# Performance work log

Measured on AMD Instinct MI355X. Metric: run time of the kernel, lower is better.

Reference implementation:

```python
import jax, jax.numpy as jnp
import numpy as np

N = 20000   # nodes
E = 200000  # edges
D = 32      # inp_dim == out_dim == emb_dim
R = 100     # num_rel
EPS = 1e-5  # BatchNorm1d default eps


def setup_inputs() -> dict:
    key = jax.random.key(0)
    ks = jax.random.split(key, 5)
    h = jax.random.normal(ks[0], (N, D), dtype=jnp.float32)
    # xavier_uniform-ish scale for [R, D, D] relation weights
    weight = jax.random.normal(ks[1], (R, D, D), dtype=jnp.float32) * (1.0 / np.sqrt(D))
    gamma = jnp.ones((D,), dtype=jnp.float32)
    beta = jnp.zeros((D,), dtype=jnp.float32)
    src = jax.random.randint(ks[2], (E,), 0, N, dtype=jnp.int32)
    dst = jax.random.randint(ks[3], (E,), 0, N, dtype=jnp.int32)
    etype = jax.random.randint(ks[4], (E,), 0, R, dtype=jnp.int32)
    return {"h": h, "weight": weight, "gamma": gamma, "beta": beta,
            "src": src, "dst": dst, "etype": etype}


def reference(h, weight, gamma, beta, src, dst, etype):
    # per-edge relation-weight gather: [E, D, D]
    w_e = weight[etype]
    # per-edge bmm (src feature row-vector @ relation matrix) + relu: [E, D]
    msg = jax.nn.relu(jnp.einsum('ed,edo->eo', h[src], w_e))
    # BatchNorm1d in training mode: batch stats over the edge dimension
    mu = jnp.mean(msg, axis=0)
    var = jnp.mean(jnp.square(msg - mu), axis=0)  # biased variance
    msg = (msg - mu) * jax.lax.rsqrt(var + EPS) * gamma + beta
    # segment-mean reduce of messages into destination nodes: [N, D]
    ssum = jax.ops.segment_sum(msg, dst, num_segments=N)
    cnt = jax.ops.segment_sum(jnp.ones((E,), msg.dtype), dst, num_segments=N)
    return ssum / jnp.maximum(cnt, 1.0)[:, None]
```

## Files before the change

### kernel.cpp

```cpp
#include <hip/hip_runtime.h>

#define D 32
#define EPS 1e-5f
#define TPB 256
#define NB 256
#define RNB_MAX 25600
#define SCAN_T 1024

__global__ void histE_kernel(const int* __restrict__ etype, const int* __restrict__ dst,
                             int E, int R, int chunk,
                             int* __restrict__ blockHistT,
                             int* __restrict__ nodeCnt)
{
    __shared__ int lh[1024];
    for (int i = threadIdx.x; i < R; i += TPB) lh[i] = 0;
    __syncthreads();
    const int lo = blockIdx.x * chunk, hi = min(E, lo + chunk);
    for (int e = lo + threadIdx.x; e < hi; e += TPB) {
        atomicAdd(&lh[etype[e]], 1);
        atomicAdd(&nodeCnt[dst[e]], 1);
    }
    __syncthreads();
    for (int r = threadIdx.x; r < R; r += TPB)
        blockHistT[r * NB + blockIdx.x] = lh[r];
}

__global__ __launch_bounds__(SCAN_T)
void scanAll_kernel(int* __restrict__ blockHistT, int R,
                    const int* __restrict__ nodeCnt, int N, int E,
                    int* __restrict__ rel_start,
                    int* __restrict__ task_rel, int* __restrict__ task_start,
                    int* __restrict__ n_tasks,
                    int* __restrict__ node_start, int* __restrict__ curD)
{
    __shared__ int s_buf[RNB_MAX];
    __shared__ int s_part[SCAN_T];
    __shared__ int s_tbase[1024];
    const int t = threadIdx.x;

    const int M = R * NB;
    for (int i = t; i < M; i += SCAN_T) s_buf[i] = blockHistT[i];
    __syncthreads();
    {
        const int per = (M + SCAN_T - 1) / SCAN_T;
        const int lo = min(t * per, M), hi = min(lo + per, M);
        int s = 0;
        for (int i = lo; i < hi; ++i) s += s_buf[i];
        s_part[t] = s;
        __syncthreads();
        int x = s;
        for (int off = 1; off < SCAN_T; off <<= 1) {
            const int y = (t >= off) ? s_part[t - off] : 0;
            __syncthreads();
            x += y;
            s_part[t] = x;
            __syncthreads();
        }
        int run = x - s;
        for (int i = lo; i < hi; ++i) { const int v = s_buf[i]; s_buf[i] = run; run += v; }
    }
    __syncthreads();
    for (int i = t; i < M; i += SCAN_T) blockHistT[i] = s_buf[i];
    for (int r = t; r < R; r += SCAN_T) rel_start[r] = s_buf[r * NB];
    if (t == 0) rel_start[R] = E;
    if (t == 0) {
        int tb = 0;
        for (int r = 0; r < R; ++r) {
            const int st  = s_buf[r * NB];
            const int en  = (r + 1 < R) ? s_buf[(r + 1) * NB] : E;
            s_tbase[r] = tb;
            tb += (en - st + TPB - 1) / TPB;
        }
        *n_tasks = tb;
    }
    __syncthreads();
    if (t < R) {
        const int st = s_buf[t * NB];
        const int en = (t + 1 < R) ? s_buf[(t + 1) * NB] : E;
        const int nb = (en - st + TPB - 1) / TPB;
        const int tb = s_tbase[t];
        for (int b = 0; b < nb; ++b) {
            task_rel[tb + b]   = t;
            task_start[tb + b] = st + b * TPB;
        }
    }
    __syncthreads();

    for (int i = t; i < N; i += SCAN_T) s_buf[i] = nodeCnt[i];
    __syncthreads();
    {
        const int per = (N + SCAN_T - 1) / SCAN_T;
        const int lo = min(t * per, N), hi = min(lo + per, N);
        int s = 0;
        for (int i = lo; i < hi; ++i) s += s_buf[i];
        s_part[t] = s;
        __syncthreads();
        int x = s;
        for (int off = 1; off < SCAN_T; off <<= 1) {
            const int y = (t >= off) ? s_part[t - off] : 0;
            __syncthreads();
            x += y;
            s_part[t] = x;
            __syncthreads();
        }
        int run = x - s;
        for (int i = lo; i < hi; ++i) { const int v = s_buf[i]; s_buf[i] = run; run += v; }
    }
    __syncthreads();
    for (int i = t; i < N; i += SCAN_T) {
        const int v = s_buf[i];
        node_start[i] = v;
        curD[i] = v;
    }
    if (t == 0) node_start[N] = E;
}

__global__ void scatterE_kernel(const int* __restrict__ src, const int* __restrict__ dst,
                                const int* __restrict__ etype, int E, int R, int chunk,
                                const int* __restrict__ blockHistT,
                                int* __restrict__ ssrc, int* __restrict__ sdst)
{
    __shared__ int cur[1024];
    for (int r = threadIdx.x; r < R; r += TPB)
        cur[r] = blockHistT[r * NB + blockIdx.x];
    __syncthreads();
    const int lo = blockIdx.x * chunk, hi = min(E, lo + chunk);
    for (int e = lo + threadIdx.x; e < hi; e += TPB) {
        const int p = atomicAdd(&cur[etype[e]], 1);
        ssrc[p] = src[e];
        sdst[p] = dst[e];
    }
}

__global__ __launch_bounds__(TPB)
void rgcn_compute(const float* __restrict__ h, const float* __restrict__ W,
                  const int* __restrict__ rel_start,
                  const int* __restrict__ task_rel, const int* __restrict__ task_start,
                  const int* __restrict__ n_tasks_p,
                  const int* __restrict__ ssrc, const int* __restrict__ sdst,
                  int* __restrict__ curD,
                  float* __restrict__ msg,
                  float* __restrict__ stat_sum, float* __restrict__ stat_sq)
{
    __shared__ float s_tile[TPB * 33];
    __shared__ int   s_src[TPB];
    __shared__ int   s_pos[TPB];
    __shared__ float s_aux[2 * TPB];

    const int task = blockIdx.x;
    if (task >= *n_tasks_p) return;
    const int r      = task_rel[task];
    const int start  = task_start[task];
    const int relEnd = rel_start[r + 1];
    const int nE     = min(TPB, relEnd - start);
    const int tid    = threadIdx.x;

    if (tid < nE) {
        s_src[tid] = ssrc[start + tid];
        s_pos[tid] = atomicAdd(&curD[sdst[start + tid]], 1);
    }
    __syncthreads();

    for (int i = tid; i < nE * 8; i += TPB) {
        const int row = i >> 3, seg = i & 7;
        const float4 v = *(const float4*)(h + (size_t)s_src[row] * D + seg * 4);
        float* p = &s_tile[row * 33 + seg * 4];
        p[0] = v.x; p[1] = v.y; p[2] = v.z; p[3] = v.w;
    }
    __syncthreads();

    const float* Wr = W + (size_t)__builtin_amdgcn_readfirstlane(r) * (D * D);

    float acc[D];
#pragma unroll
    for (int o = 0; o < D; ++o) acc[o] = 0.f;

    if (tid < nE) {
#pragma unroll 4
        for (int d = 0; d < D; ++d) {
            const float hd = s_tile[tid * 33 + d];
#pragma unroll
            for (int o = 0; o < D; ++o)
                acc[o] = fmaf(hd, Wr[d * D + o], acc[o]);
        }
#pragma unroll
        for (int o = 0; o < D; ++o) acc[o] = fmaxf(acc[o], 0.f);
    }
    __syncthreads();

    if (tid < nE) {
#pragma unroll
        for (int o = 0; o < D; ++o) s_tile[tid * 33 + o] = acc[o];
    }
    __syncthreads();

    float ps = 0.f, pq = 0.f;
    for (int i = tid; i < nE * D; i += TPB) {
        const int row = i >> 5, o = i & 31;
        const float v = s_tile[row * 33 + o];
        msg[(size_t)s_pos[row] * D + o] = v;
        ps += v; pq += v * v;
    }
    s_aux[tid]       = ps;
    s_aux[TPB + tid] = pq;
    __syncthreads();
    if (tid < D) {
        float ss = 0.f, sq = 0.f;
#pragma unroll
        for (int c = 0; c < TPB / D; ++c) {
            ss += s_aux[c * D + tid];
            sq += s_aux[TPB + c * D + tid];
        }
        atomicAdd(&stat_sum[tid], ss);
        atomicAdd(&stat_sq[tid],  sq);
    }
}

__global__ void reduce_kernel(const float* __restrict__ msg,
                              const int* __restrict__ node_start,
                              const float* __restrict__ stat_sum,
                              const float* __restrict__ stat_sq,
                              const float* __restrict__ gamma,
                              const float* __restrict__ beta,
                              float invE, float* __restrict__ out, int N)
{
    const int o = threadIdx.x & 31;
    const int n = blockIdx.x * 8 + (threadIdx.x >> 5);
    if (n >= N) return;
    const int j0 = node_start[n], j1 = node_start[n + 1];
    float s = 0.f;
    for (int j = j0; j < j1; ++j)
        s += msg[(size_t)j * D + o];
    const float mu  = stat_sum[o] * invE;
    const float var = fmaxf(stat_sq[o] * invE - mu * mu, 0.f);
    const float is  = rsqrtf(var + EPS);
    const float sc  = gamma[o] * is;
    const float sh  = fmaf(-mu, sc, beta[o]);
    const float c   = (float)(j1 - j0);
    out[(size_t)n * D + o] = fmaf(s, sc, sh * c) / fmaxf(c, 1.0f);
}

extern "C" void kernel_launch(void* const* d_in, const int* in_sizes, int n_in,
                              void* d_out, int out_size, void* d_ws, size_t ws_size,
                              hipStream_t stream)
{
    const float* h     = (const float*)d_in[0];
    const float* W     = (const float*)d_in[1];
    const float* gamma = (const float*)d_in[2];
    const float* beta  = (const float*)d_in[3];
    const int*   src   = (const int*)d_in[4];
    const int*   dst   = (const int*)d_in[5];
    const int*   etype = (const int*)d_in[6];
    float* out = (float*)d_out;

    const int E = in_sizes[4];
    const int N = in_sizes[0] / D;
    const int R = in_sizes[1] / (D * D);
    const int T = R + (E + TPB - 1) / TPB;
    const int chunk = (E + NB - 1) / NB;

    int*   nodeCnt   = (int*)d_ws;
    float* stat_sum  = (float*)(nodeCnt + N);
    float* stat_sq   = stat_sum + D;
    int*   node_start= (int*)(stat_sq + D);
    int*   curD      = node_start + N + 1;
    int*   rel_start = curD + N;
    int*   n_tasks   = rel_start + R + 1;
    int*   blockHistT= n_tasks + 1;
    int*   task_rel  = blockHistT + R * NB;
    int*   task_start= task_rel + T;
    int*   ssrc      = task_start + T;
    int*   sdst      = ssrc + E;
    float* msg       = (float*)(sdst + E);

    hipMemsetAsync(d_ws, 0, sizeof(int) * (size_t)(N + 2 * D), stream);

    histE_kernel<<<NB, TPB, 0, stream>>>(etype, dst, E, R, chunk, blockHistT, nodeCnt);
    scanAll_kernel<<<1, SCAN_T, 0, stream>>>(blockHistT, R, nodeCnt, N, E,
                                             rel_start, task_rel, task_start, n_tasks,
                                             node_start, curD);
    scatterE_kernel<<<NB, TPB, 0, stream>>>(src, dst, etype, E, R, chunk,
                                            blockHistT, ssrc, sdst);
    rgcn_compute<<<T, TPB, 0, stream>>>(h, W, rel_start, task_rel, task_start,
                                        n_tasks, ssrc, sdst, curD,
                                        msg, stat_sum, stat_sq);
    reduce_kernel<<<(N + 7) / 8, TPB, 0, stream>>>(msg, node_start,
                                                   stat_sum, stat_sq, gamma, beta,
                                                   1.0f / (float)E, out, N);
}
```

Baseline: 156.2 us.

## Spread BN stat atomics, finalize stats via last-block ticket, pack edges

BatchNorm statistic accumulation now goes to 32 replicated copies instead of one pair of counters, which cuts atomic contention on the 64 global addresses. The last compute block, found through a ticket counter, folds the copies into per-channel scale and shift. The reduce kernel then only applies those values. Source and destination indices are packed into one int2 array, and the serial task-base loop in the scan kernel becomes a parallel 128-wide scan. These changes add a thread fence and an extra atomic per block, and the 128-wide scan assumes R <= 128.

```diff
diff --git a/kernel.cpp b/kernel.cpp
--- a/kernel.cpp
+++ b/kernel.cpp
@@ -6,6 +6,7 @@
 #define NB 256
 #define RNB_MAX 25600
 #define SCAN_T 1024
+#define SC 32
 
 __global__ void histE_kernel(const int* __restrict__ etype, const int* __restrict__ dst,
                              int E, int R, int chunk,
@@ -35,7 +36,6 @@
 {
     __shared__ int s_buf[RNB_MAX];
     __shared__ int s_part[SCAN_T];
-    __shared__ int s_tbase[1024];
     const int t = threadIdx.x;
 
     const int M = R * NB;
@@ -63,25 +63,28 @@
     for (int i = t; i < M; i += SCAN_T) blockHistT[i] = s_buf[i];
     for (int r = t; r < R; r += SCAN_T) rel_start[r] = s_buf[r * NB];
     if (t == 0) rel_start[R] = E;
-    if (t == 0) {
-        int tb = 0;
-        for (int r = 0; r < R; ++r) {
-            const int st  = s_buf[r * NB];
-            const int en  = (r + 1 < R) ? s_buf[(r + 1) * NB] : E;
-            s_tbase[r] = tb;
-            tb += (en - st + TPB - 1) / TPB;
-        }
-        *n_tasks = tb;
-    }
-    __syncthreads();
+
+    int nbv = 0, stv = 0;
     if (t < R) {
-        const int st = s_buf[t * NB];
+        stv = s_buf[t * NB];
         const int en = (t + 1 < R) ? s_buf[(t + 1) * NB] : E;
-        const int nb = (en - st + TPB - 1) / TPB;
-        const int tb = s_tbase[t];
-        for (int b = 0; b < nb; ++b) {
+        nbv = (en - stv + TPB - 1) / TPB;
+    }
+    if (t < 128) s_part[t] = nbv;
+    __syncthreads();
+    for (int off = 1; off < 128; off <<= 1) {
+        int y = 0;
+        if (t < 128 && t >= off) y = s_part[t - off];
+        __syncthreads();
+        if (t < 128) s_part[t] += y;
+        __syncthreads();
+    }
+    if (t == R - 1) *n_tasks = s_part[t];
+    if (t < R) {
+        const int tb = s_part[t] - nbv;
+        for (int b = 0; b < nbv; ++b) {
             task_rel[tb + b]   = t;
-            task_start[tb + b] = st + b * TPB;
+            task_start[tb + b] = stv + b * TPB;
         }
     }
     __syncthreads();
@@ -118,7 +121,7 @@
 __global__ void scatterE_kernel(const int* __restrict__ src, const int* __restrict__ dst,
                                 const int* __restrict__ etype, int E, int R, int chunk,
                                 const int* __restrict__ blockHistT,
-                                int* __restrict__ ssrc, int* __restrict__ sdst)
+                                int2* __restrict__ sedge)
 {
     __shared__ int cur[1024];
     for (int r = threadIdx.x; r < R; r += TPB)
@@ -126,9 +129,9 @@
     __syncthreads();
     const int lo = blockIdx.x * chunk, hi = min(E, lo + chunk);
     for (int e = lo + threadIdx.x; e < hi; e += TPB) {
+        const int2 v = make_int2(src[e], dst[e]);
         const int p = atomicAdd(&cur[etype[e]], 1);
-        ssrc[p] = src[e];
-        sdst[p] = dst[e];
+        sedge[p] = v;
     }
 }
 
@@ -137,18 +140,24 @@
                   const int* __restrict__ rel_start,
                   const int* __restrict__ task_rel, const int* __restrict__ task_start,
                   const int* __restrict__ n_tasks_p,
-                  const int* __restrict__ ssrc, const int* __restrict__ sdst,
+                  const int2* __restrict__ sedge,
                   int* __restrict__ curD,
                   float* __restrict__ msg,
-                  float* __restrict__ stat_sum, float* __restrict__ stat_sq)
+                  float* __restrict__ statC,
+                  int* __restrict__ ticket,
+                  const float* __restrict__ gamma, const float* __restrict__ beta,
+                  float invE,
+                  float* __restrict__ scale, float* __restrict__ shift)
 {
     __shared__ float s_tile[TPB * 33];
     __shared__ int   s_src[TPB];
     __shared__ int   s_pos[TPB];
     __shared__ float s_aux[2 * TPB];
-
+    __shared__ int   s_last;
+
+    const int nTasks = *n_tasks_p;
     const int task = blockIdx.x;
-    if (task >= *n_tasks_p) return;
+    if (task >= nTasks) return;
     const int r      = task_rel[task];
     const int start  = task_start[task];
     const int relEnd = rel_start[r + 1];
@@ -156,8 +165,9 @@
     const int tid    = threadIdx.x;
 
     if (tid < nE) {
-        s_src[tid] = ssrc[start + tid];
-        s_pos[tid] = atomicAdd(&curD[sdst[start + tid]], 1);
+        const int2 ed = sedge[start + tid];
+        s_src[tid] = ed.x;
+        s_pos[tid] = atomicAdd(&curD[ed.y], 1);
     }
     __syncthreads();
 
@@ -204,6 +214,7 @@
     s_aux[tid]       = ps;
     s_aux[TPB + tid] = pq;
     __syncthreads();
+    const int copy = task & (SC - 1);
     if (tid < D) {
         float ss = 0.f, sq = 0.f;
 #pragma unroll
@@ -211,18 +222,34 @@
             ss += s_aux[c * D + tid];
             sq += s_aux[TPB + c * D + tid];
         }
-        atomicAdd(&stat_sum[tid], ss);
-        atomicAdd(&stat_sq[tid],  sq);
+        atomicAdd(&statC[copy * D + tid], ss);
+        atomicAdd(&statC[SC * D + copy * D + tid], sq);
+    }
+
+    __threadfence();
+    __syncthreads();
+    if (tid == 0) s_last = atomicAdd(ticket, 1);
+    __syncthreads();
+    if (s_last == nTasks - 1 && tid < D) {
+        float ssum = 0.f, ssq = 0.f;
+        for (int c = 0; c < SC; ++c) {
+            ssum += atomicAdd(&statC[c * D + tid], 0.0f);
+            ssq  += atomicAdd(&statC[SC * D + c * D + tid], 0.0f);
+        }
+        const float mu  = ssum * invE;
+        const float var = fmaxf(ssq * invE - mu * mu, 0.f);
+        const float is  = rsqrtf(var + EPS);
+        const float sc  = gamma[tid] * is;
+        scale[tid] = sc;
+        shift[tid] = fmaf(-mu, sc, beta[tid]);
     }
 }
 
 __global__ void reduce_kernel(const float* __restrict__ msg,
                               const int* __restrict__ node_start,
-                              const float* __restrict__ stat_sum,
-                              const float* __restrict__ stat_sq,
-                              const float* __restrict__ gamma,
-                              const float* __restrict__ beta,
-                              float invE, float* __restrict__ out, int N)
+                              const float* __restrict__ scale,
+                              const float* __restrict__ shift,
+                              float* __restrict__ out, int N)
 {
     const int o = threadIdx.x & 31;
     const int n = blockIdx.x * 8 + (threadIdx.x >> 5);
@@ -231,13 +258,8 @@
     float s = 0.f;
     for (int j = j0; j < j1; ++j)
         s += msg[(size_t)j * D + o];
-    const float mu  = stat_sum[o] * invE;
-    const float var = fmaxf(stat_sq[o] * invE - mu * mu, 0.f);
-    const float is  = rsqrtf(var + EPS);
-    const float sc  = gamma[o] * is;
-    const float sh  = fmaf(-mu, sc, beta[o]);
-    const float c   = (float)(j1 - j0);
-    out[(size_t)n * D + o] = fmaf(s, sc, sh * c) / fmaxf(c, 1.0f);
+    const float c = (float)(j1 - j0);
+    out[(size_t)n * D + o] = fmaf(s, scale[o], shift[o] * c) / fmaxf(c, 1.0f);
 }
 
 extern "C" void kernel_launch(void* const* d_in, const int* in_sizes, int n_in,
@@ -260,31 +282,34 @@
     const int chunk = (E + NB - 1) / NB;
 
     int*   nodeCnt   = (int*)d_ws;
-    float* stat_sum  = (float*)(nodeCnt + N);
-    float* stat_sq   = stat_sum + D;
-    int*   node_start= (int*)(stat_sq + D);
+    float* statC     = (float*)(nodeCnt + N);
+    int*   ticket    = (int*)(statC + 2 * SC * D);
+    float* scale     = (float*)(ticket + 1);
+    float* shift     = scale + D;
+    int*   node_start= (int*)(shift + D);
     int*   curD      = node_start + N + 1;
     int*   rel_start = curD + N;
     int*   n_tasks   = rel_start + R + 1;
     int*   blockHistT= n_tasks + 1;
     int*   task_rel  = blockHistT + R * NB;
     int*   task_start= task_rel + T;
-    int*   ssrc      = task_start + T;
-    int*   sdst      = ssrc + E;
-    float* msg       = (float*)(sdst + E);
-
-    hipMemsetAsync(d_ws, 0, sizeof(int) * (size_t)(N + 2 * D), stream);
+    int*   pend      = task_start + T;
+    if (((uintptr_t)pend) & 7) pend++;
+    int2*  sedge     = (int2*)pend;
+    float* msg       = (float*)(sedge + E);
+
+    hipMemsetAsync(d_ws, 0, sizeof(int) * (size_t)(N + 2 * SC * D + 1), stream);
 
     histE_kernel<<<NB, TPB, 0, stream>>>(etype, dst, E, R, chunk, blockHistT, nodeCnt);
     scanAll_kernel<<<1, SCAN_T, 0, stream>>>(blockHistT, R, nodeCnt, N, E,
                                              rel_start, task_rel, task_start, n_tasks,
                                              node_start, curD);
     scatterE_kernel<<<NB, TPB, 0, stream>>>(src, dst, etype, E, R, chunk,
-                                            blockHistT, ssrc, sdst);
+                                            blockHistT, sedge);
     rgcn_compute<<<T, TPB, 0, stream>>>(h, W, rel_start, task_rel, task_start,
-                                        n_tasks, ssrc, sdst, curD,
-                                        msg, stat_sum, stat_sq);
+                                        n_tasks, sedge, curD, msg,
+                                        statC, ticket, gamma, beta,
+                                        1.0f / (float)E, scale, shift);
     reduce_kernel<<<(N + 7) / 8, TPB, 0, stream>>>(msg, node_start,
-                                                   stat_sum, stat_sq, gamma, beta,
-                                                   1.0f / (float)E, out, N);
-}
+                                                   scale, shift, out, N);
+}
```

After: 256.8 us. 1.64x slower.
